# Performance work log

Measured on AMD Instinct MI355X. Metric: run time of the kernel, lower is better.

Reference implementation:

```python
import jax, jax.numpy as jnp
import numpy as np

LATENT = 512
VOCAB = 32000
START_TOKEN = 0
END_TOKEN = 1
BATCH = 128
BN_EPS = 1e-5


def setup_inputs() -> dict:
    key = jax.random.key(0)
    k = jax.random.split(key, 10)
    s = 0.02
    L, V = LATENT, VOCAB
    return {
        "z": jax.random.normal(k[0], (BATCH, L), dtype=jnp.float32),
        "emb": jax.random.normal(k[1], (V, L), dtype=jnp.float32) * s,      # embedding table
        "Wp1": jax.random.normal(k[2], (2 * L, L), dtype=jnp.float32) * s,  # project layer 1
        "bp1": jnp.zeros((2 * L,), jnp.float32),
        "Wp2": jax.random.normal(k[3], (2 * L, 2 * L), dtype=jnp.float32) * s,  # project layer 2
        "bp2": jnp.zeros((2 * L,), jnp.float32),
        "Wih": jax.random.normal(k[4], (4 * L, L), dtype=jnp.float32) * s,  # LSTMCell input weights (i,f,g,o)
        "Whh": jax.random.normal(k[5], (4 * L, L), dtype=jnp.float32) * s,
        "bih": jnp.zeros((4 * L,), jnp.float32),
        "bhh": jnp.zeros((4 * L,), jnp.float32),
        "Wo1": jax.random.normal(k[6], (2 * L, L), dtype=jnp.float32) * s,  # output MLP layer 1
        "bo1": jnp.zeros((2 * L,), jnp.float32),
        "bn_g": jnp.ones((2 * L,), jnp.float32),   # BatchNorm1d (eval mode)
        "bn_b": jnp.zeros((2 * L,), jnp.float32),
        "bn_m": jnp.zeros((2 * L,), jnp.float32),
        "bn_v": jnp.ones((2 * L,), jnp.float32),
        "Wo2": jax.random.normal(k[7], (V - 1, 2 * L), dtype=jnp.float32) * s,  # vocab head
        "bo2": jnp.zeros((V - 1,), jnp.float32),
        "max_len": 50,
    }


def _elu01(x):
    # nn.ELU(alpha=0.1)
    return jnp.where(x > 0, x, 0.1 * (jnp.exp(x) - 1.0))


def _run(z, emb, Wp1, bp1, Wp2, bp2, Wih, Whh, bih, bhh,
         Wo1, bo1, bn_g, bn_b, bn_m, bn_v, Wo2, bo2, max_len):
    B, L = z.shape
    # project z -> (h, c); dropout inactive in eval mode
    h1 = jax.nn.relu(z @ Wp1.T + bp1)
    hc = _elu01(h1 @ Wp2.T + bp2)
    h, c = jnp.split(hc, 2, axis=1)            # each [B, L]
    e0 = jnp.broadcast_to(emb[START_TOKEN], (B, L))
    keys = jax.random.split(jax.random.key(42), max_len)
    inv_std = bn_g / jnp.sqrt(bn_v + BN_EPS)   # fused BN scale (eval)

    def step(carry, key):
        h, c, e = carry
        gates = e @ Wih.T + bih + h @ Whh.T + bhh
        i, f, g, o = jnp.split(gates, 4, axis=1)  # torch LSTMCell gate order
        c = jax.nn.sigmoid(f) * c + jax.nn.sigmoid(i) * jnp.tanh(g)
        h = jax.nn.sigmoid(o) * jnp.tanh(c)
        a = jax.nn.relu(h) @ Wo1.T + bo1
        a = (a - bn_m) * inv_std + bn_b
        logits = jax.nn.relu(a) @ Wo2.T + bo2      # [B, V-1]
        logp = jax.nn.log_softmax(logits, axis=-1)
        # Categorical sampling via Gumbel-max
        sample = jnp.argmax(logits + jax.random.gumbel(key, logits.shape), axis=-1)
        lp = jnp.take_along_axis(logp, sample[:, None], axis=1)[:, 0]
        ent = -jnp.sum(jnp.exp(logp) * logp, axis=-1)
        return (h, c, jnp.take(emb, sample, axis=0)), (sample, lp, ent)

    _, (xs, lps, ents) = jax.lax.scan(step, (h, c, e0), keys)
    x = xs.T          # [B, T]
    lps = lps.T       # [B, T]
    ents = ents.T     # [B, T]
    # first END occurrence (argmax returns first max; replicates torch semantics incl. its length-1 quirk)
    end_pos = jnp.argmax((x == END_TOKEN).astype(jnp.float32), axis=1)
    seq_len = end_pos + 1
    seq_len = jnp.where(seq_len == 1, max_len, seq_len)
    mask = jnp.arange(max_len)[None, :] < seq_len[:, None]
    x_out = jnp.where(mask, x + 1, 0)                      # pad_sequence(padding=-1) then +1 -> 0 pad
    lp_out = jnp.where(mask, lps, 0.0)                     # padded per-step log-probs
    ent_mean = jnp.sum(jnp.where(mask, ents, 0.0), axis=1) / seq_len.astype(ents.dtype)
    return x_out, lp_out, ent_mean


def reference(z, emb, Wp1, bp1, Wp2, bp2, Wih, Whh, bih, bhh,
              Wo1, bo1, bn_g, bn_b, bn_m, bn_v, Wo2, bo2, max_len):
    return _run(z, emb, Wp1, bp1, Wp2, bp2, Wih, Whh, bih, bhh,
                Wo1, bo1, bn_g, bn_b, bn_m, bn_v, Wo2, bo2, max_len)
```

## Files before the change

kernel.cpp:

```cpp
#include <hip/hip_runtime.h>
#include <stdint.h>
#include <math.h>

#define BATCH  128
#define NV     31999
#define NSTEP  50
#define NPB    500
#define TINYF  1.17549435e-38f

typedef __attribute__((ext_vector_type(8))) short bf16x8;
typedef __attribute__((ext_vector_type(4))) float f32x4;
typedef __attribute__((ext_vector_type(4))) unsigned int u32x4;

__host__ __device__ __forceinline__ void tf2x32(uint32_t k0, uint32_t k1,
                                                uint32_t x0, uint32_t x1,
                                                uint32_t& o0, uint32_t& o1) {
  uint32_t k2 = k0 ^ k1 ^ 0x1BD11BDAu;
  x0 += k0; x1 += k1;
#define TF_R(r) { x0 += x1; x1 = (x1 << (r)) | (x1 >> (32 - (r))); x1 ^= x0; }
  TF_R(13) TF_R(15) TF_R(26) TF_R(6)
  x0 += k1; x1 += k2 + 1u;
  TF_R(17) TF_R(29) TF_R(16) TF_R(24)
  x0 += k2; x1 += k0 + 2u;
  TF_R(13) TF_R(15) TF_R(26) TF_R(6)
  x0 += k0; x1 += k1 + 3u;
  TF_R(17) TF_R(29) TF_R(16) TF_R(24)
  x0 += k1; x1 += k2 + 4u;
  TF_R(13) TF_R(15) TF_R(26) TF_R(6)
  x0 += k2; x1 += k0 + 5u;
#undef TF_R
  o0 = x0; o1 = x1;
}

__device__ __forceinline__ float sigm(float x) { return 1.0f / (1.0f + expf(-x)); }

__device__ __forceinline__ float gumbelv(uint32_t k0, uint32_t k1, uint32_t f) {
  uint32_t o0, o1; tf2x32(k0, k1, 0u, f, o0, o1);
  uint32_t bits = o0 ^ o1;
  float ff = __uint_as_float((bits >> 9) | 0x3f800000u) - 1.0f;
  float u = ff + TINYF;
  return -logf(-logf(u));
}

__device__ __forceinline__ unsigned short bfhi(float x) {
  uint32_t u = __float_as_uint(x);
  u += 0x7fffu + ((u >> 16) & 1u);
  return (unsigned short)(u >> 16);
}
__device__ __forceinline__ void split2(float x, unsigned short& h, unsigned short& l) {
  unsigned short hh = bfhi(x);
  float hf = __uint_as_float(((uint32_t)hh) << 16);
  h = hh; l = bfhi(x - hf);
}

#define MFMA3(ah, al, bh, bl, c)                                            \
  c = __builtin_amdgcn_mfma_f32_16x16x32_bf16(ah, bh, c, 0, 0, 0);          \
  c = __builtin_amdgcn_mfma_f32_16x16x32_bf16(ah, bl, c, 0, 0, 0);          \
  c = __builtin_amdgcn_mfma_f32_16x16x32_bf16(al, bh, c, 0, 0, 0);

__global__ __launch_bounds__(256) void gemm_part(
    const float* __restrict__ A, int lda,
    const float* __restrict__ Wa, const float* __restrict__ Wb,
    int ks, int K, int N, int KC, float* __restrict__ part)
{
  __shared__ float As[32][132];
  __shared__ float Ws[32][68];
  const int tx = threadIdx.x;
  const int n0 = blockIdx.x * 64;
  const int kc = blockIdx.y;
  const int cg = tx & 15, rg = tx >> 4;
  float acc[8][4] = {};
  const int kend = (kc + 1) * KC;
  for (int kk = kc * KC; kk < kend; kk += 32) {
    __syncthreads();
#pragma unroll
    for (int i = 0; i < 16; ++i) {
      int e = tx + 256 * i; int b = e >> 5, k = e & 31;
      As[k][b] = A[b * lda + kk + k];
    }
#pragma unroll
    for (int i = 0; i < 8; ++i) {
      int e = tx + 256 * i; int n = e >> 5, k = e & 31;
      int nn = n0 + n, kg = kk + k;
      float w;
      if (kg < ks) w = Wa[(size_t)nn * ks + kg];
      else         w = Wb[(size_t)nn * (K - ks) + (kg - ks)];
      Ws[k][n] = w;
    }
    __syncthreads();
#pragma unroll
    for (int k = 0; k < 32; ++k) {
      float4 a0 = *(const float4*)&As[k][rg * 8];
      float4 a1 = *(const float4*)&As[k][rg * 8 + 4];
      float4 wv = *(const float4*)&Ws[k][cg * 4];
      float ar[8] = {a0.x, a0.y, a0.z, a0.w, a1.x, a1.y, a1.z, a1.w};
      float wr[4] = {wv.x, wv.y, wv.z, wv.w};
#pragma unroll
      for (int r = 0; r < 8; ++r)
#pragma unroll
        for (int c = 0; c < 4; ++c) acc[r][c] += ar[r] * wr[c];
    }
  }
  size_t base = (size_t)kc * BATCH * N;
#pragma unroll
  for (int r = 0; r < 8; ++r) {
    int row = rg * 8 + r;
    float4 v4 = make_float4(acc[r][0], acc[r][1], acc[r][2], acc[r][3]);
    *(float4*)&part[base + (size_t)row * N + n0 + cg * 4] = v4;
  }
}

__global__ void k_reduce_relu(const float* __restrict__ part, int nkc,
                              const float* __restrict__ bias,
                              float* __restrict__ out, int N) {
  int i = blockIdx.x * 256 + threadIdx.x;
  int n = i % N;
  float s = bias[n];
  for (int kc = 0; kc < nkc; ++kc) s += part[(size_t)kc * BATCH * N + i];
  out[i] = fmaxf(s, 0.0f);
}

__global__ void k_reduce_elu_split(const float* __restrict__ part, int nkc,
                                   const float* __restrict__ bias,
                                   unsigned short* __restrict__ xh,
                                   unsigned short* __restrict__ xl,
                                   float* __restrict__ cbuf) {
  int i = blockIdx.x * 256 + threadIdx.x;
  int b = i >> 10, n = i & 1023;
  float s = bias[n];
  for (int kc = 0; kc < nkc; ++kc) s += part[(size_t)kc * BATCH * 1024 + i];
  float e = (s > 0.0f) ? s : 0.1f * (expf(s) - 1.0f);
  if (n < 512) {
    unsigned short h_, l_; split2(e, h_, l_);
    xh[b * 1024 + 512 + n] = h_; xl[b * 1024 + 512 + n] = l_;
  } else cbuf[b * 512 + (n - 512)] = e;
}

__global__ void k_fill_e0(const float* __restrict__ emb,
                          unsigned short* __restrict__ xh,
                          unsigned short* __restrict__ xl) {
  int i = blockIdx.x * 256 + threadIdx.x;
  int b = i >> 9, k = i & 511;
  unsigned short h_, l_; split2(emb[k], h_, l_);
  xh[b * 1024 + k] = h_; xl[b * 1024 + k] = l_;
}

__global__ void k_prep_gates(const float* __restrict__ Wih, const float* __restrict__ Whh,
                             const float* __restrict__ bih, const float* __restrict__ bhh,
                             unsigned short* __restrict__ Wh, unsigned short* __restrict__ Wl,
                             float* __restrict__ bg) {
  int i = blockIdx.x * 256 + threadIdx.x;
  int idx8 = i * 8;
  int n = idx8 >> 10, k0 = idx8 & 1023;
  const float* src = (k0 < 512) ? (Wih + (size_t)n * 512 + k0)
                                : (Whh + (size_t)n * 512 + (k0 - 512));
  float4 a = *(const float4*)src, b = *(const float4*)(src + 4);
  float wv[8] = {a.x, a.y, a.z, a.w, b.x, b.y, b.z, b.w};
  unsigned short hh[8], ll[8];
#pragma unroll
  for (int q = 0; q < 8; ++q) split2(wv[q], hh[q], ll[q]);
  u32x4 h4, l4;
#pragma unroll
  for (int q = 0; q < 4; ++q) {
    h4[q] = (uint32_t)hh[2 * q] | ((uint32_t)hh[2 * q + 1] << 16);
    l4[q] = (uint32_t)ll[2 * q] | ((uint32_t)ll[2 * q + 1] << 16);
  }
  *(u32x4*)(Wh + (size_t)idx8) = h4;
  *(u32x4*)(Wl + (size_t)idx8) = l4;
  if (i < 256) {
#pragma unroll
    for (int q = 0; q < 8; ++q) bg[i * 8 + q] = bih[i * 8 + q] + bhh[i * 8 + q];
  }
}

__global__ void k_prep_out1(const float* __restrict__ Wo1, const float* __restrict__ bo1,
                            const float* __restrict__ g, const float* __restrict__ bb,
                            const float* __restrict__ m, const float* __restrict__ v,
                            unsigned short* __restrict__ Wh, unsigned short* __restrict__ Wl,
                            float* __restrict__ S, float* __restrict__ T) {
  int i = blockIdx.x * 256 + threadIdx.x;
  int idx8 = i * 8;
  float4 a = *(const float4*)(Wo1 + idx8), b = *(const float4*)(Wo1 + idx8 + 4);
  float wv[8] = {a.x, a.y, a.z, a.w, b.x, b.y, b.z, b.w};
  unsigned short hh[8], ll[8];
#pragma unroll
  for (int q = 0; q < 8; ++q) split2(wv[q], hh[q], ll[q]);
  u32x4 h4, l4;
#pragma unroll
  for (int q = 0; q < 4; ++q) {
    h4[q] = (uint32_t)hh[2 * q] | ((uint32_t)hh[2 * q + 1] << 16);
    l4[q] = (uint32_t)ll[2 * q] | ((uint32_t)ll[2 * q + 1] << 16);
  }
  *(u32x4*)(Wh + (size_t)idx8) = h4;
  *(u32x4*)(Wl + (size_t)idx8) = l4;
  if (i < 128) {
#pragma unroll
    for (int q = 0; q < 8; ++q) {
      int n = i * 8 + q;
      float s = g[n] / sqrtf(v[n] + 1e-5f);
      S[n] = s;
      T[n] = (bo1[n] - m[n]) * s + bb[n];
    }
  }
}

__global__ void k_prep_wo2(const float* __restrict__ W,
                           unsigned short* __restrict__ Wh, unsigned short* __restrict__ Wl,
                           int total8) {
  int i = blockIdx.x * 256 + threadIdx.x;
  if (i >= total8) return;
  const float* wp = W + (size_t)i * 8;
  float4 a = *(const float4*)wp, b = *(const float4*)(wp + 4);
  float wv[8] = {a.x, a.y, a.z, a.w, b.x, b.y, b.z, b.w};
  unsigned short hh[8], ll[8];
#pragma unroll
  for (int q = 0; q < 8; ++q) split2(wv[q], hh[q], ll[q]);
  u32x4 h4, l4;
#pragma unroll
  for (int q = 0; q < 4; ++q) {
    h4[q] = (uint32_t)hh[2 * q] | ((uint32_t)hh[2 * q + 1] << 16);
    l4[q] = (uint32_t)ll[2 * q] | ((uint32_t)ll[2 * q + 1] << 16);
  }
  *(u32x4*)(Wh + (size_t)i * 8) = h4;
  *(u32x4*)(Wl + (size_t)i * 8) = l4;
}


__global__ __launch_bounds__(256) void k_gates(
    const unsigned short* __restrict__ Ah, const unsigned short* __restrict__ Al,
    const unsigned short* __restrict__ Wh, const unsigned short* __restrict__ Wl,
    const float* __restrict__ bg, float* __restrict__ cbuf,
    unsigned short* __restrict__ xh, unsigned short* __restrict__ xl,
    unsigned short* __restrict__ rhh, unsigned short* __restrict__ rhl)
{
  __shared__ __align__(16) unsigned char SM[40960];
  unsigned short (*WHb)[2][64][40] = (unsigned short(*)[2][64][40])SM;
  unsigned short (*WLb)[2][64][40] = (unsigned short(*)[2][64][40])(SM + 20480);
  const int tx = threadIdx.x;
  const int lane = tx & 63, w = tx >> 6;
  const int l15 = lane & 15, g4 = lane >> 4;
  const int gblk = blockIdx.x;
  const int arow0 = w * 32 + l15, ak = g4 * 8;
  const int sr = tx >> 2, sq = tx & 3;
  const int grow = (sr >> 4) * 512 + gblk * 16 + (sr & 15);
  const size_t wbase = (size_t)grow * 1024;

  f32x4 acc[2][4] = {};
  u32x4 RH[2][2], RL[2][2];
  bf16x8 QH[2][2][2], QL[2][2][2];

  auto ldW = [&](int set, int t) {
    const int kk = t * 64 + sq * 16;
    RH[set][0] = *(const u32x4*)(Wh + wbase + kk);
    RH[set][1] = *(const u32x4*)(Wh + wbase + kk + 8);
    RL[set][0] = *(const u32x4*)(Wl + wbase + kk);
    RL[set][1] = *(const u32x4*)(Wl + wbase + kk + 8);
  };
  auto stW = [&](int set, int buf) {
    const int kc = sq >> 1, ko = (sq & 1) * 16;
    *(u32x4*)&WHb[buf][kc][sr][ko]     = RH[set][0];
    *(u32x4*)&WHb[buf][kc][sr][ko + 8] = RH[set][1];
    *(u32x4*)&WLb[buf][kc][sr][ko]     = RL[set][0];
    *(u32x4*)&WLb[buf][kc][sr][ko + 8] = RL[set][1];
  };
  auto ldA = [&](int set, int t) {
#pragma unroll
    for (int rf = 0; rf < 2; ++rf)
#pragma unroll
      for (int kc = 0; kc < 2; ++kc) {
        size_t ao = (size_t)(arow0 + rf * 16) * 1024 + t * 64 + kc * 32 + ak;
        QH[set][rf][kc] = *(const bf16x8*)(Ah + ao);
        QL[set][rf][kc] = *(const bf16x8*)(Al + ao);
      }
  };
  auto comp = [&](int buf, int set) {
#pragma unroll
    for (int kc = 0; kc < 2; ++kc)
#pragma unroll
      for (int cf = 0; cf < 4; ++cf) {
        int col = cf * 16 + l15;
        bf16x8 bh = *(const bf16x8*)&WHb[buf][kc][col][ak];
        bf16x8 bl = *(const bf16x8*)&WLb[buf][kc][col][ak];
#pragma unroll
        for (int rf = 0; rf < 2; ++rf) { MFMA3(QH[set][rf][kc], QL[set][rf][kc], bh, bl, acc[rf][cf]); }
      }
  };

  ldW(0, 0); ldW(1, 1); ldA(0, 0);
  stW(0, 0); __syncthreads();
  for (int t = 0; t < 16; ++t) {
    const int pb = t & 1;
    if (t < 14) ldW(pb, t + 2);
    if (t < 15) ldA(pb ^ 1, t + 1);
    comp(pb, pb);
    if (t < 15) stW(pb ^ 1, pb ^ 1);
    __syncthreads();
  }
  float* gex = (float*)SM;
#pragma unroll
  for (int rf = 0; rf < 2; ++rf)
#pragma unroll
    for (int cf = 0; cf < 4; ++cf)
#pragma unroll
      for (int r = 0; r < 4; ++r) {
        int brow = w * 32 + rf * 16 + g4 * 4 + r;
        gex[(cf * 128 + brow) * 17 + l15] = acc[rf][cf][r];
      }
  __syncthreads();
#pragma unroll
  for (int i = 0; i < 8; ++i) {
    int e = tx + 256 * i;
    int b = e >> 4, lj = e & 15;
    int jg = gblk * 16 + lj;
    float gi = gex[(0 * 128 + b) * 17 + lj] + bg[jg];
    float gf = gex[(1 * 128 + b) * 17 + lj] + bg[512 + jg];
    float gg = gex[(2 * 128 + b) * 17 + lj] + bg[1024 + jg];
    float go = gex[(3 * 128 + b) * 17 + lj] + bg[1536 + jg];
    float co = cbuf[b * 512 + jg];
    float cn = sigm(gf) * co + sigm(gi) * tanhf(gg);
    float hn = sigm(go) * tanhf(cn);
    cbuf[b * 512 + jg] = cn;
    unsigned short h_, l_;
    split2(hn, h_, l_);
    xh[b * 1024 + 512 + jg] = h_; xl[b * 1024 + 512 + jg] = l_;
    float r = fmaxf(hn, 0.0f);
    split2(r, h_, l_);
    rhh[b * 512 + jg] = h_; rhl[b * 512 + jg] = l_;
  }
}

__global__ __launch_bounds__(256) void k_out1(
    const unsigned short* __restrict__ Ah, const unsigned short* __restrict__ Al,
    const unsigned short* __restrict__ Wh, const unsigned short* __restrict__ Wl,
    const float* __restrict__ S, const float* __restrict__ T,
    unsigned short* __restrict__ r2h, unsigned short* __restrict__ r2l)
{
  __shared__ __align__(16) unsigned char SM[40960];
  unsigned short (*WHb)[2][64][40] = (unsigned short(*)[2][64][40])SM;
  unsigned short (*WLb)[2][64][40] = (unsigned short(*)[2][64][40])(SM + 20480);
  const int tx = threadIdx.x;
  const int lane = tx & 63, w = tx >> 6;
  const int l15 = lane & 15, g4 = lane >> 4;
  const int n0 = blockIdx.x * 64;
  const int arow0 = w * 32 + l15, ak = g4 * 8;
  const int sr = tx >> 2, sq = tx & 3;
  const size_t wbase = (size_t)(n0 + sr) * 512;

  f32x4 acc[2][4] = {};
  u32x4 RH[2][2], RL[2][2];
  bf16x8 QH[2][2][2], QL[2][2][2];

  auto ldW = [&](int set, int t) {
    const int kk = t * 64 + sq * 16;
    RH[set][0] = *(const u32x4*)(Wh + wbase + kk);
    RH[set][1] = *(const u32x4*)(Wh + wbase + kk + 8);
    RL[set][0] = *(const u32x4*)(Wl + wbase + kk);
    RL[set][1] = *(const u32x4*)(Wl + wbase + kk + 8);
  };
  auto stW = [&](int set, int buf) {
    const int kc = sq >> 1, ko = (sq & 1) * 16;
    *(u32x4*)&WHb[buf][kc][sr][ko]     = RH[set][0];
    *(u32x4*)&WHb[buf][kc][sr][ko + 8] = RH[set][1];
    *(u32x4*)&WLb[buf][kc][sr][ko]     = RL[set][0];
    *(u32x4*)&WLb[buf][kc][sr][ko + 8] = RL[set][1];
  };
  auto ldA = [&](int set, int t) {
#pragma unroll
    for (int rf = 0; rf < 2; ++rf)
#pragma unroll
      for (int kc = 0; kc < 2; ++kc) {
        size_t ao = (size_t)(arow0 + rf * 16) * 512 + t * 64 + kc * 32 + ak;
        QH[set][rf][kc] = *(const bf16x8*)(Ah + ao);
        QL[set][rf][kc] = *(const bf16x8*)(Al + ao);
      }
  };
  auto comp = [&](int buf, int set) {
#pragma unroll
    for (int kc = 0; kc < 2; ++kc)
#pragma unroll
      for (int cf = 0; cf < 4; ++cf) {
        int col = cf * 16 + l15;
        bf16x8 bh = *(const bf16x8*)&WHb[buf][kc][col][ak];
        bf16x8 bl = *(const bf16x8*)&WLb[buf][kc][col][ak];
#pragma unroll
        for (int rf = 0; rf < 2; ++rf) { MFMA3(QH[set][rf][kc], QL[set][rf][kc], bh, bl, acc[rf][cf]); }
      }
  };

  ldW(0, 0); ldW(1, 1); ldA(0, 0);
  stW(0, 0); __syncthreads();
  for (int t = 0; t < 8; ++t) {
    const int pb = t & 1;
    if (t < 6) ldW(pb, t + 2);
    if (t < 7) ldA(pb ^ 1, t + 1);
    comp(pb, pb);
    if (t < 7) stW(pb ^ 1, pb ^ 1);
    __syncthreads();
  }
#pragma unroll
  for (int cf = 0; cf < 4; ++cf) {
    int n = n0 + cf * 16 + l15;
    float s = S[n], t = T[n];
#pragma unroll
    for (int rf = 0; rf < 2; ++rf)
#pragma unroll
      for (int r = 0; r < 4; ++r) {
        int row = w * 32 + rf * 16 + g4 * 4 + r;
        float v = fmaxf(acc[rf][cf][r] * s + t, 0.0f);
        unsigned short h_, l_; split2(v, h_, l_);
        r2h[row * 1024 + n] = h_; r2l[row * 1024 + n] = l_;
      }
  }
}

template<int PRE>
__global__ __launch_bounds__(256) void k_vocab(
    const unsigned short* __restrict__ Ah, const unsigned short* __restrict__ Al,
    const unsigned short* __restrict__ Wh, const unsigned short* __restrict__ Wl,
    const float* __restrict__ Wf, const float* __restrict__ bias,
    uint32_t key0, uint32_t key1,
    float* __restrict__ vpmax, float* __restrict__ vps1, float* __restrict__ vps2,
    float* __restrict__ vpbv, float* __restrict__ vpbl, int* __restrict__ vpbi)
{
  __shared__ __align__(16) unsigned char SM[40960];
  unsigned short (*WHb)[2][64][40] = (unsigned short(*)[2][64][40])SM;
  unsigned short (*WLb)[2][64][40] = (unsigned short(*)[2][64][40])(SM + 20480);
  const int tx = threadIdx.x;
  const int lane = tx & 63, w = tx >> 6;
  const int l15 = lane & 15, g4 = lane >> 4;
  const int n0 = blockIdx.x * 64;
  const int arow0 = w * 32 + l15, ak = g4 * 8;
  const int sr = tx >> 2, sq = tx & 3;
  int grow = n0 + sr; if (grow >= NV) grow = NV - 1;
  const size_t wbase = (size_t)grow * 1024;

  f32x4 acc[2][4] = {};
  u32x4 RH[2][2], RL[2][2];
  float4 RF[2][4];
  bf16x8 QH[2][2][2], QL[2][2][2];

  auto ldW = [&](int set, int t) {
    const int kk = t * 64 + sq * 16;
    if (PRE) {
      RH[set][0] = *(const u32x4*)(Wh + wbase + kk);
      RH[set][1] = *(const u32x4*)(Wh + wbase + kk + 8);
      RL[set][0] = *(const u32x4*)(Wl + wbase + kk);
      RL[set][1] = *(const u32x4*)(Wl + wbase + kk + 8);
    } else {
      const float* wp = Wf + wbase + kk;
#pragma unroll
      for (int q = 0; q < 4; ++q) RF[set][q] = *(const float4*)(wp + q * 4);
    }
  };
  auto stW = [&](int set, int buf) {
    const int kc = sq >> 1, ko = (sq & 1) * 16;
    if (PRE) {
      *(u32x4*)&WHb[buf][kc][sr][ko]     = RH[set][0];
      *(u32x4*)&WHb[buf][kc][sr][ko + 8] = RH[set][1];
      *(u32x4*)&WLb[buf][kc][sr][ko]     = RL[set][0];
      *(u32x4*)&WLb[buf][kc][sr][ko + 8] = RL[set][1];
    } else {
      unsigned short hh[16], ll[16];
#pragma unroll
      for (int q = 0; q < 4; ++q) {
        float4 f = RF[set][q];
        split2(f.x, hh[q*4], ll[q*4]);   split2(f.y, hh[q*4+1], ll[q*4+1]);
        split2(f.z, hh[q*4+2], ll[q*4+2]); split2(f.w, hh[q*4+3], ll[q*4+3]);
      }
#pragma unroll
      for (int q = 0; q < 16; ++q) { WHb[buf][kc][sr][ko+q] = hh[q]; WLb[buf][kc][sr][ko+q] = ll[q]; }
    }
  };
  auto ldA = [&](int set, int t) {
#pragma unroll
    for (int rf = 0; rf < 2; ++rf)
#pragma unroll
      for (int kc = 0; kc < 2; ++kc) {
        size_t ao = (size_t)(arow0 + rf * 16) * 1024 + t * 64 + kc * 32 + ak;
        QH[set][rf][kc] = *(const bf16x8*)(Ah + ao);
        QL[set][rf][kc] = *(const bf16x8*)(Al + ao);
      }
  };
  auto comp = [&](int buf, int set) {
#pragma unroll
    for (int kc = 0; kc < 2; ++kc)
#pragma unroll
      for (int cf = 0; cf < 4; ++cf) {
        int col = cf * 16 + l15;
        bf16x8 bh = *(const bf16x8*)&WHb[buf][kc][col][ak];
        bf16x8 bl = *(const bf16x8*)&WLb[buf][kc][col][ak];
#pragma unroll
        for (int rf = 0; rf < 2; ++rf) { MFMA3(QH[set][rf][kc], QL[set][rf][kc], bh, bl, acc[rf][cf]); }
      }
  };

  ldW(0, 0); ldW(1, 1); ldA(0, 0);
  stW(0, 0); __syncthreads();
  for (int t = 0; t < 16; ++t) {
    const int pb = t & 1;
    if (t < 14) ldW(pb, t + 2);
    if (t < 15) ldA(pb ^ 1, t + 1);
    comp(pb, pb);
    if (t < 15) stW(pb ^ 1, pb ^ 1);
    __syncthreads();
  }
  float bias_c[4]; int vcol[4];
#pragma unroll
  for (int cf = 0; cf < 4; ++cf) {
    int v = n0 + cf * 16 + l15;
    vcol[cf] = v;
    bias_c[cf] = (v < NV) ? bias[v] : 0.0f;
  }
#pragma unroll
  for (int rf = 0; rf < 2; ++rf) {
#pragma unroll
    for (int reg = 0; reg < 4; ++reg) {
      int row = w * 32 + rf * 16 + g4 * 4 + reg;
      float lv[4], pv[4];
      float mm = -INFINITY;
#pragma unroll
      for (int cf = 0; cf < 4; ++cf) {
        if (vcol[cf] < NV) {
          float l = acc[rf][cf][reg] + bias_c[cf];
          float g = gumbelv(key0, key1, (uint32_t)row * 31999u + (uint32_t)vcol[cf]);
          lv[cf] = l; pv[cf] = l + g;
          mm = fmaxf(mm, l);
        } else { lv[cf] = -INFINITY; pv[cf] = -INFINITY; }
      }
      for (int d = 1; d <= 8; d <<= 1) mm = fmaxf(mm, __shfl_xor(mm, d));
      float s1 = 0.0f, s2 = 0.0f;
#pragma unroll
      for (int cf = 0; cf < 4; ++cf)
        if (vcol[cf] < NV) { float t = lv[cf] - mm; float e = expf(t); s1 += e; s2 += e * t; }
      for (int d = 1; d <= 8; d <<= 1) { s1 += __shfl_xor(s1, d); s2 += __shfl_xor(s2, d); }
      float bv = -INFINITY, bl_ = 0.0f; int bi = 0x7fffffff;
#pragma unroll
      for (int cf = 0; cf < 4; ++cf)
        if (pv[cf] > bv || (pv[cf] == bv && vcol[cf] < bi)) { bv = pv[cf]; bi = vcol[cf]; bl_ = lv[cf]; }
      for (int d = 1; d <= 8; d <<= 1) {
        float ov = __shfl_xor(bv, d); int oi = __shfl_xor(bi, d); float ol = __shfl_xor(bl_, d);
        if (ov > bv || (ov == bv && oi < bi)) { bv = ov; bi = oi; bl_ = ol; }
      }
      if (l15 == 0) {
        int o = row * NPB + blockIdx.x;
        vpmax[o] = mm; vps1[o] = s1; vps2[o] = s2;
        vpbv[o] = bv; vpbl[o] = bl_; vpbi[o] = bi;
      }
    }
  }
}

__global__ void k_final_sample(const float* __restrict__ vpmax, const float* __restrict__ vps1,
                               const float* __restrict__ vps2, const float* __restrict__ vpbv,
                               const float* __restrict__ vpbl, const int* __restrict__ vpbi,
                               int t, int* __restrict__ xhist, float* __restrict__ lph,
                               float* __restrict__ enth, const float* __restrict__ emb,
                               unsigned short* __restrict__ xh, unsigned short* __restrict__ xl) {
  int b = blockIdx.x, lane = threadIdx.x;
  float M = -INFINITY;
  for (int p = lane; p < NPB; p += 64) M = fmaxf(M, vpmax[b * NPB + p]);
  for (int d = 32; d; d >>= 1) M = fmaxf(M, __shfl_xor(M, d));
  float S1 = 0.0f, S2 = 0.0f, bv = -INFINITY, bl = 0.0f; int bi = 0x7fffffff;
  for (int p = lane; p < NPB; p += 64) {
    int o = b * NPB + p;
    float dm = vpmax[o] - M;
    float sc = expf(dm);
    S1 += vps1[o] * sc;
    S2 += (vps2[o] + dm * vps1[o]) * sc;
    float v = vpbv[o]; int ii = vpbi[o];
    if (v > bv || (v == bv && ii < bi)) { bv = v; bi = ii; bl = vpbl[o]; }
  }
  for (int d = 32; d; d >>= 1) {
    S1 += __shfl_xor(S1, d); S2 += __shfl_xor(S2, d);
    float ov = __shfl_xor(bv, d); int oi = __shfl_xor(bi, d); float ol = __shfl_xor(bl, d);
    if (ov > bv || (ov == bv && oi < bi)) { bv = ov; bi = oi; bl = ol; }
  }
  float logZ = logf(S1);
  if (lane == 0) {
    xhist[t * 128 + b] = bi;
    lph[t * 128 + b] = bl - M - logZ;
    enth[t * 128 + b] = logZ - S2 / S1;
  }
  const float* er = emb + (size_t)bi * 512;
  for (int k = lane; k < 512; k += 64) {
    unsigned short h_, l_; split2(er[k], h_, l_);
    xh[b * 1024 + k] = h_; xl[b * 1024 + k] = l_;
  }
}

__global__ void k_finalize(const int* __restrict__ xhist, const float* __restrict__ lph,
                           const float* __restrict__ enth, float* __restrict__ out) {
  int b = blockIdx.x, lane = threadIdx.x;
  int tok = -1, cand = 1 << 20;
  if (lane < NSTEP) {
    tok = xhist[lane * 128 + b];
    if (tok == 1) cand = lane;
  }
  int e = cand;
  for (int d = 32; d; d >>= 1) e = min(e, __shfl_xor(e, d));
  int end_pos = (e >= (1 << 20)) ? 0 : e;
  int seq_len = end_pos + 1;
  if (seq_len == 1) seq_len = NSTEP;
  float ent = 0.0f;
  if (lane < NSTEP) {
    bool msk = lane < seq_len;
    out[b * NSTEP + lane]        = msk ? (float)(tok + 1) : 0.0f;
    out[6400 + b * NSTEP + lane] = msk ? lph[lane * 128 + b] : 0.0f;
    ent = msk ? enth[lane * 128 + b] : 0.0f;
  }
  for (int d = 32; d; d >>= 1) ent += __shfl_xor(ent, d);
  if (lane == 0) out[12800 + b] = ent / (float)seq_len;
}

extern "C" void kernel_launch(void* const* d_in, const int* in_sizes, int n_in,
                              void* d_out, int out_size, void* d_ws, size_t ws_size,
                              hipStream_t stream) {
  const float* z    = (const float*)d_in[0];
  const float* emb  = (const float*)d_in[1];
  const float* Wp1  = (const float*)d_in[2];
  const float* bp1  = (const float*)d_in[3];
  const float* Wp2  = (const float*)d_in[4];
  const float* bp2  = (const float*)d_in[5];
  const float* Wih  = (const float*)d_in[6];
  const float* Whh  = (const float*)d_in[7];
  const float* bih  = (const float*)d_in[8];
  const float* bhh  = (const float*)d_in[9];
  const float* Wo1  = (const float*)d_in[10];
  const float* bo1  = (const float*)d_in[11];
  const float* bng  = (const float*)d_in[12];
  const float* bnb  = (const float*)d_in[13];
  const float* bnm  = (const float*)d_in[14];
  const float* bnv  = (const float*)d_in[15];
  const float* Wo2  = (const float*)d_in[16];
  const float* bo2  = (const float*)d_in[17];
  float* out = (float*)d_out;
  (void)in_sizes; (void)n_in; (void)out_size;

  char* base = (char*)d_ws;
  size_t off = 0;
  auto alloc = [&](size_t bytes) -> void* {
    void* p = base + off;
    off = (off + bytes + 255) & ~(size_t)255;
    return p;
  };
  unsigned short* xh[2]; unsigned short* xl[2];
  xh[0] = (unsigned short*)alloc(128 * 1024 * 2);
  xl[0] = (unsigned short*)alloc(128 * 1024 * 2);
  xh[1] = (unsigned short*)alloc(128 * 1024 * 2);
  xl[1] = (unsigned short*)alloc(128 * 1024 * 2);
  float* cbuf = (float*)alloc(128 * 512 * 4);
  unsigned short* rhh = (unsigned short*)alloc(128 * 512 * 2);
  unsigned short* rhl = (unsigned short*)alloc(128 * 512 * 2);
  unsigned short* r2h = (unsigned short*)alloc(128 * 1024 * 2);
  unsigned short* r2l = (unsigned short*)alloc(128 * 1024 * 2);
  float* h1    = (float*)alloc(128 * 1024 * 4);
  float* apart = (float*)alloc((size_t)8 * 128 * 1024 * 4);
  unsigned short* Wgh = (unsigned short*)alloc((size_t)2048 * 1024 * 2);
  unsigned short* Wgl = (unsigned short*)alloc((size_t)2048 * 1024 * 2);
  float* bg = (float*)alloc(2048 * 4);
  unsigned short* Wo1h = (unsigned short*)alloc((size_t)1024 * 512 * 2);
  unsigned short* Wo1l = (unsigned short*)alloc((size_t)1024 * 512 * 2);
  float* Sbn = (float*)alloc(1024 * 4);
  float* Tbn = (float*)alloc(1024 * 4);
  float* vpmax = (float*)alloc((size_t)NPB * 128 * 4);
  float* vps1  = (float*)alloc((size_t)NPB * 128 * 4);
  float* vps2  = (float*)alloc((size_t)NPB * 128 * 4);
  float* vpbv  = (float*)alloc((size_t)NPB * 128 * 4);
  float* vpbl  = (float*)alloc((size_t)NPB * 128 * 4);
  int*   vpbi  = (int*)alloc((size_t)NPB * 128 * 4);
  int*   xhist = (int*)alloc(50 * 128 * 4);
  float* lph   = (float*)alloc(50 * 128 * 4);
  float* enth  = (float*)alloc(50 * 128 * 4);
  size_t wo2_elems = (size_t)NV * 1024;
  bool pre = ws_size >= off + 2 * wo2_elems * 2 + (1 << 20);
  unsigned short* Wo2h = nullptr; unsigned short* Wo2l = nullptr;
  if (pre) {
    Wo2h = (unsigned short*)alloc(wo2_elems * 2);
    Wo2l = (unsigned short*)alloc(wo2_elems * 2);
  }

  uint32_t outk[100];
  for (int t = 0; t < 50; ++t) {
    uint32_t y0, y1;
    tf2x32(0u, 42u, 0u, (uint32_t)t, y0, y1);
    outk[2 * t] = y0; outk[2 * t + 1] = y1;
  }

  k_prep_gates<<<1024, 256, 0, stream>>>(Wih, Whh, bih, bhh, Wgh, Wgl, bg);
  k_prep_out1<<<256, 256, 0, stream>>>(Wo1, bo1, bng, bnb, bnm, bnv, Wo1h, Wo1l, Sbn, Tbn);
  if (pre) {
    int total8 = (int)(wo2_elems / 8);
    k_prep_wo2<<<(total8 + 255) / 256, 256, 0, stream>>>(Wo2, Wo2h, Wo2l, total8);
  }

  k_fill_e0<<<256, 256, 0, stream>>>(emb, xh[0], xl[0]);
  gemm_part<<<dim3(16, 4), 256, 0, stream>>>(z, 512, Wp1, Wp1, 512, 512, 1024, 128, apart);
  k_reduce_relu<<<512, 256, 0, stream>>>(apart, 4, bp1, h1, 1024);
  gemm_part<<<dim3(16, 8), 256, 0, stream>>>(h1, 1024, Wp2, Wp2, 1024, 1024, 1024, 128, apart);
  k_reduce_elu_split<<<512, 256, 0, stream>>>(apart, 8, bp2, xh[0], xl[0], cbuf);

  for (int t = 0; t < NSTEP; ++t) {
    int ri = t & 1, wi = ri ^ 1;
    k_gates<<<32, 256, 0, stream>>>(xh[ri], xl[ri], Wgh, Wgl, bg, cbuf,
                                    xh[wi], xl[wi], rhh, rhl);
    k_out1<<<16, 256, 0, stream>>>(rhh, rhl, Wo1h, Wo1l, Sbn, Tbn, r2h, r2l);
    if (pre)
      k_vocab<1><<<NPB, 256, 0, stream>>>(r2h, r2l, Wo2h, Wo2l, Wo2, bo2,
                                          outk[2 * t], outk[2 * t + 1],
                                          vpmax, vps1, vps2, vpbv, vpbl, vpbi);
    else
      k_vocab<0><<<NPB, 256, 0, stream>>>(r2h, r2l, nullptr, nullptr, Wo2, bo2,
                                          outk[2 * t], outk[2 * t + 1],
                                          vpmax, vps1, vps2, vpbv, vpbl, vpbi);
    k_final_sample<<<128, 64, 0, stream>>>(vpmax, vps1, vps2, vpbv, vpbl, vpbi,
                                           t, xhist, lph, enth, emb, xh[wi], xl[wi]);
  }
  k_finalize<<<128, 64, 0, stream>>>(xhist, lph, enth, out);
}
```

Measured before the change: 5.249 ms.

## Use 512-thread vocab blocks with 16 rows per wave and triple-buffered weight loads

The vocab head kernel moves from 256 to 512 threads per block. Each of the 8 waves now covers 16 batch rows instead of 32, and each thread stages 8 weight elements per tile instead of 16. Weight prefetch deepens from 2 to 3 register sets, with launch bounds requesting 4 waves per SIMD. The aim is more waves in flight to hide latency on the memory-bound vocab GEMM, at the cost of smaller per-wave tiles and more shared-memory B-fragment reads per MFMA.

New measurement: 4.828 ms. 1.09x faster.

```diff
diff --git a/kernel.cpp b/kernel.cpp
--- a/kernel.cpp
+++ b/kernel.cpp
@@ -225,7 +225,6 @@
   *(u32x4*)(Wl + (size_t)i * 8) = l4;
 }
 
-
 __global__ __launch_bounds__(256) void k_gates(
     const unsigned short* __restrict__ Ah, const unsigned short* __restrict__ Al,
     const unsigned short* __restrict__ Wh, const unsigned short* __restrict__ Wl,
@@ -414,7 +413,7 @@
 }
 
 template<int PRE>
-__global__ __launch_bounds__(256) void k_vocab(
+__global__ __launch_bounds__(512, 4) void k_vocab(
     const unsigned short* __restrict__ Ah, const unsigned short* __restrict__ Al,
     const unsigned short* __restrict__ Wh, const unsigned short* __restrict__ Wl,
     const float* __restrict__ Wf, const float* __restrict__ bias,
@@ -429,59 +428,50 @@
   const int lane = tx & 63, w = tx >> 6;
   const int l15 = lane & 15, g4 = lane >> 4;
   const int n0 = blockIdx.x * 64;
-  const int arow0 = w * 32 + l15, ak = g4 * 8;
-  const int sr = tx >> 2, sq = tx & 3;
+  const int arow = w * 16 + l15, ak = g4 * 8;
+  const int sr = tx >> 3, sq = tx & 7;
   int grow = n0 + sr; if (grow >= NV) grow = NV - 1;
   const size_t wbase = (size_t)grow * 1024;
-
-  f32x4 acc[2][4] = {};
-  u32x4 RH[2][2], RL[2][2];
-  float4 RF[2][4];
-  bf16x8 QH[2][2][2], QL[2][2][2];
-
-  auto ldW = [&](int set, int t) {
-    const int kk = t * 64 + sq * 16;
+  const int skc = sq >> 2, sko = (sq & 3) * 8;
+
+  f32x4 acc[4] = {};
+  u32x4 RH[3], RL[3];
+  float4 RF[3][2];
+  bf16x8 QH[2][2], QL[2][2];
+
+  auto ldW = [&](int s, int t) {
+    const int kk = t * 64 + sq * 8;
     if (PRE) {
-      RH[set][0] = *(const u32x4*)(Wh + wbase + kk);
-      RH[set][1] = *(const u32x4*)(Wh + wbase + kk + 8);
-      RL[set][0] = *(const u32x4*)(Wl + wbase + kk);
-      RL[set][1] = *(const u32x4*)(Wl + wbase + kk + 8);
+      RH[s] = *(const u32x4*)(Wh + wbase + kk);
+      RL[s] = *(const u32x4*)(Wl + wbase + kk);
     } else {
-      const float* wp = Wf + wbase + kk;
-#pragma unroll
-      for (int q = 0; q < 4; ++q) RF[set][q] = *(const float4*)(wp + q * 4);
-    }
-  };
-  auto stW = [&](int set, int buf) {
-    const int kc = sq >> 1, ko = (sq & 1) * 16;
+      RF[s][0] = *(const float4*)(Wf + wbase + kk);
+      RF[s][1] = *(const float4*)(Wf + wbase + kk + 4);
+    }
+  };
+  auto stW = [&](int s, int buf) {
     if (PRE) {
-      *(u32x4*)&WHb[buf][kc][sr][ko]     = RH[set][0];
-      *(u32x4*)&WHb[buf][kc][sr][ko + 8] = RH[set][1];
-      *(u32x4*)&WLb[buf][kc][sr][ko]     = RL[set][0];
-      *(u32x4*)&WLb[buf][kc][sr][ko + 8] = RL[set][1];
+      *(u32x4*)&WHb[buf][skc][sr][sko] = RH[s];
+      *(u32x4*)&WLb[buf][skc][sr][sko] = RL[s];
     } else {
-      unsigned short hh[16], ll[16];
-#pragma unroll
-      for (int q = 0; q < 4; ++q) {
-        float4 f = RF[set][q];
-        split2(f.x, hh[q*4], ll[q*4]);   split2(f.y, hh[q*4+1], ll[q*4+1]);
-        split2(f.z, hh[q*4+2], ll[q*4+2]); split2(f.w, hh[q*4+3], ll[q*4+3]);
-      }
-#pragma unroll
-      for (int q = 0; q < 16; ++q) { WHb[buf][kc][sr][ko+q] = hh[q]; WLb[buf][kc][sr][ko+q] = ll[q]; }
-    }
-  };
-  auto ldA = [&](int set, int t) {
-#pragma unroll
-    for (int rf = 0; rf < 2; ++rf)
-#pragma unroll
-      for (int kc = 0; kc < 2; ++kc) {
-        size_t ao = (size_t)(arow0 + rf * 16) * 1024 + t * 64 + kc * 32 + ak;
-        QH[set][rf][kc] = *(const bf16x8*)(Ah + ao);
-        QL[set][rf][kc] = *(const bf16x8*)(Al + ao);
-      }
-  };
-  auto comp = [&](int buf, int set) {
+      float fv[8] = {RF[s][0].x, RF[s][0].y, RF[s][0].z, RF[s][0].w,
+                     RF[s][1].x, RF[s][1].y, RF[s][1].z, RF[s][1].w};
+      unsigned short hh[8], ll[8];
+#pragma unroll
+      for (int q = 0; q < 8; ++q) split2(fv[q], hh[q], ll[q]);
+#pragma unroll
+      for (int q = 0; q < 8; ++q) { WHb[buf][skc][sr][sko + q] = hh[q]; WLb[buf][skc][sr][sko + q] = ll[q]; }
+    }
+  };
+  auto ldA = [&](int s, int t) {
+#pragma unroll
+    for (int kc = 0; kc < 2; ++kc) {
+      size_t ao = (size_t)arow * 1024 + t * 64 + kc * 32 + ak;
+      QH[s][kc] = *(const bf16x8*)(Ah + ao);
+      QL[s][kc] = *(const bf16x8*)(Al + ao);
+    }
+  };
+  auto comp = [&](int buf, int s) {
 #pragma unroll
     for (int kc = 0; kc < 2; ++kc)
 #pragma unroll
@@ -489,19 +479,18 @@
         int col = cf * 16 + l15;
         bf16x8 bh = *(const bf16x8*)&WHb[buf][kc][col][ak];
         bf16x8 bl = *(const bf16x8*)&WLb[buf][kc][col][ak];
-#pragma unroll
-        for (int rf = 0; rf < 2; ++rf) { MFMA3(QH[set][rf][kc], QL[set][rf][kc], bh, bl, acc[rf][cf]); }
+        MFMA3(QH[s][kc], QL[s][kc], bh, bl, acc[cf]);
       }
   };
 
-  ldW(0, 0); ldW(1, 1); ldA(0, 0);
+  ldW(0, 0); ldW(1, 1); ldW(2, 2); ldA(0, 0);
   stW(0, 0); __syncthreads();
   for (int t = 0; t < 16; ++t) {
     const int pb = t & 1;
-    if (t < 14) ldW(pb, t + 2);
-    if (t < 15) ldA(pb ^ 1, t + 1);
-    comp(pb, pb);
-    if (t < 15) stW(pb ^ 1, pb ^ 1);
+    if (t < 13) ldW(t % 3, t + 3);
+    if (t < 15) ldA((t + 1) & 1, t + 1);
+    comp(pb, t & 1);
+    if (t < 15) stW((t + 1) % 3, pb ^ 1);
     __syncthreads();
   }
   float bias_c[4]; int vcol[4];
@@ -512,40 +501,37 @@
     bias_c[cf] = (v < NV) ? bias[v] : 0.0f;
   }
 #pragma unroll
-  for (int rf = 0; rf < 2; ++rf) {
-#pragma unroll
-    for (int reg = 0; reg < 4; ++reg) {
-      int row = w * 32 + rf * 16 + g4 * 4 + reg;
-      float lv[4], pv[4];
-      float mm = -INFINITY;
-#pragma unroll
-      for (int cf = 0; cf < 4; ++cf) {
-        if (vcol[cf] < NV) {
-          float l = acc[rf][cf][reg] + bias_c[cf];
-          float g = gumbelv(key0, key1, (uint32_t)row * 31999u + (uint32_t)vcol[cf]);
-          lv[cf] = l; pv[cf] = l + g;
-          mm = fmaxf(mm, l);
-        } else { lv[cf] = -INFINITY; pv[cf] = -INFINITY; }
-      }
-      for (int d = 1; d <= 8; d <<= 1) mm = fmaxf(mm, __shfl_xor(mm, d));
-      float s1 = 0.0f, s2 = 0.0f;
-#pragma unroll
-      for (int cf = 0; cf < 4; ++cf)
-        if (vcol[cf] < NV) { float t = lv[cf] - mm; float e = expf(t); s1 += e; s2 += e * t; }
-      for (int d = 1; d <= 8; d <<= 1) { s1 += __shfl_xor(s1, d); s2 += __shfl_xor(s2, d); }
-      float bv = -INFINITY, bl_ = 0.0f; int bi = 0x7fffffff;
-#pragma unroll
-      for (int cf = 0; cf < 4; ++cf)
-        if (pv[cf] > bv || (pv[cf] == bv && vcol[cf] < bi)) { bv = pv[cf]; bi = vcol[cf]; bl_ = lv[cf]; }
-      for (int d = 1; d <= 8; d <<= 1) {
-        float ov = __shfl_xor(bv, d); int oi = __shfl_xor(bi, d); float ol = __shfl_xor(bl_, d);
-        if (ov > bv || (ov == bv && oi < bi)) { bv = ov; bi = oi; bl_ = ol; }
-      }
-      if (l15 == 0) {
-        int o = row * NPB + blockIdx.x;
-        vpmax[o] = mm; vps1[o] = s1; vps2[o] = s2;
-        vpbv[o] = bv; vpbl[o] = bl_; vpbi[o] = bi;
-      }
+  for (int reg = 0; reg < 4; ++reg) {
+    int row = w * 16 + g4 * 4 + reg;
+    float lv[4], pv[4];
+    float mm = -INFINITY;
+#pragma unroll
+    for (int cf = 0; cf < 4; ++cf) {
+      if (vcol[cf] < NV) {
+        float l = acc[cf][reg] + bias_c[cf];
+        float g = gumbelv(key0, key1, (uint32_t)row * 31999u + (uint32_t)vcol[cf]);
+        lv[cf] = l; pv[cf] = l + g;
+        mm = fmaxf(mm, l);
+      } else { lv[cf] = -INFINITY; pv[cf] = -INFINITY; }
+    }
+    for (int d = 1; d <= 8; d <<= 1) mm = fmaxf(mm, __shfl_xor(mm, d));
+    float s1 = 0.0f, s2 = 0.0f;
+#pragma unroll
+    for (int cf = 0; cf < 4; ++cf)
+      if (vcol[cf] < NV) { float t = lv[cf] - mm; float e = expf(t); s1 += e; s2 += e * t; }
+    for (int d = 1; d <= 8; d <<= 1) { s1 += __shfl_xor(s1, d); s2 += __shfl_xor(s2, d); }
+    float bv = -INFINITY, bl_ = 0.0f; int bi = 0x7fffffff;
+#pragma unroll
+    for (int cf = 0; cf < 4; ++cf)
+      if (pv[cf] > bv || (pv[cf] == bv && vcol[cf] < bi)) { bv = pv[cf]; bi = vcol[cf]; bl_ = lv[cf]; }
+    for (int d = 1; d <= 8; d <<= 1) {
+      float ov = __shfl_xor(bv, d); int oi = __shfl_xor(bi, d); float ol = __shfl_xor(bl_, d);
+      if (ov > bv || (ov == bv && oi < bi)) { bv = ov; bi = oi; bl_ = ol; }
+    }
+    if (l15 == 0) {
+      int o = row * NPB + blockIdx.x;
+      vpmax[o] = mm; vps1[o] = s1; vps2[o] = s2;
+      vpbv[o] = bv; vpbl[o] = bl_; vpbi[o] = bi;
     }
   }
 }
@@ -705,11 +691,11 @@
                                     xh[wi], xl[wi], rhh, rhl);
     k_out1<<<16, 256, 0, stream>>>(rhh, rhl, Wo1h, Wo1l, Sbn, Tbn, r2h, r2l);
     if (pre)
-      k_vocab<1><<<NPB, 256, 0, stream>>>(r2h, r2l, Wo2h, Wo2l, Wo2, bo2,
+      k_vocab<1><<<NPB, 512, 0, stream>>>(r2h, r2l, Wo2h, Wo2l, Wo2, bo2,
                                           outk[2 * t], outk[2 * t + 1],
                                           vpmax, vps1, vps2, vpbv, vpbl, vpbi);
     else
-      k_vocab<0><<<NPB, 256, 0, stream>>>(r2h, r2l, nullptr, nullptr, Wo2, bo2,
+      k_vocab<0><<<NPB, 512, 0, stream>>>(r2h, r2l, nullptr, nullptr, Wo2, bo2,
                                           outk[2 * t], outk[2 * t + 1],
                                           vpmax, vps1, vps2, vpbv, vpbl, vpbi);
     k_final_sample<<<128, 64, 0, stream>>>(vpmax, vps1, vps2, vpbv, vpbl, vpbi,
```
